# Kernel tuning notes

Measured on AMD Instinct MI355X. Metric: run time of the kernel, lower is better.

The kernel has to match this reference:

```python
import jax, jax.numpy as jnp
import numpy as np

T = 0.1  # temperature (init arg t)


def setup_inputs() -> dict:
    key = jax.random.key(0)
    k0, k1, k2, k3 = jax.random.split(key, 4)
    B, C, H, W, N = 1, 64, 256, 256, 4096
    emb_0 = jax.random.normal(k0, (B, C, H, W), dtype=jnp.float32)
    emb_1 = jax.random.normal(k1, (B, C, H, W), dtype=jnp.float32)
    # module assumes embeddings are already L2-normalized along channels
    emb_0 = emb_0 / jnp.linalg.norm(emb_0, axis=1, keepdims=True)
    emb_1 = emb_1 / jnp.linalg.norm(emb_1, axis=1, keepdims=True)
    locations_0 = jax.random.randint(k2, (B, N, 2), 0, H).astype(jnp.float32)
    locations_1 = jax.random.randint(k3, (B, N, 2), 0, H).astype(jnp.float32)
    return {"emb_0": emb_0, "emb_1": emb_1,
            "locations_0": locations_0, "locations_1": locations_1}


def reference(emb_0, emb_1, locations_0, locations_1):
    b, c, H, W = emb_0.shape  # b == 1
    n = locations_0.shape[1]
    v = H * W
    # (b, v, c)
    e0 = emb_0.reshape(b, c, v).transpose(0, 2, 1)
    e1 = emb_1.reshape(b, c, v).transpose(0, 2, 1)
    # flatten 2D coords to linear indices: strides [W, 1]
    ind_kernel = jnp.array([W, 1], dtype=jnp.float32)
    ind_0 = (jnp.floor(locations_0) @ ind_kernel).astype(jnp.int32)[0]  # (n,)
    ind_1 = (jnp.floor(locations_1) @ ind_kernel).astype(jnp.int32)[0]  # (n,)
    e0 = e0[:, ind_0, :]  # (b, n, c)
    e1 = e1[:, ind_1, :]  # (b, n, c)
    emb = jnp.concatenate([e0, e1], axis=1)  # (b, 2n, c)
    sim = jnp.einsum('bic,bjc->bij', emb, emb)  # (b, 2n, 2n)
    exp = jnp.exp(sim / T)
    sum_e = jnp.sum(exp, axis=2) - np.exp(1.0 / T)  # subtract self-similarity
    u = jnp.arange(n)
    w = u + n
    e_uv = exp[:, u, w]  # (b, n) positive pairs
    loss = -jnp.sum(jnp.log(e_uv / sum_e[:, u]) + jnp.log(e_uv / sum_e[:, w]))
    return loss / (2 * n)
```

## Files before the change

kernel.cpp:

```cpp
#include <hip/hip_runtime.h>
#include <math.h>

#define HW2     65536
#define NLOC    4096
#define NROW    8192
#define CDIM    64
#define TINV    10.0f
#define EXP10   22026.465794806718f
#define JCHUNKS 16
#define JCHUNK  512

#if __has_builtin(__builtin_amdgcn_exp2f)
#define ASCALE  14.426950408889634f
#define EXPFN(x) __builtin_amdgcn_exp2f(x)
#else
#define ASCALE  10.0f
#define EXPFN(x) __expf(x)
#endif

typedef __attribute__((ext_vector_type(8))) short bf16x8;
typedef __attribute__((ext_vector_type(4))) float f32x4;
typedef unsigned short u16;

__device__ __forceinline__ unsigned short f2bf(float f) {
  unsigned u = __builtin_bit_cast(unsigned, f);
  u += 0x7FFFu + ((u >> 16) & 1u);
  return (unsigned short)(u >> 16);
}
__device__ __forceinline__ float bf2f(unsigned u16v) {
  unsigned u = u16v << 16;
  return __builtin_bit_cast(float, u);
}

__global__ __launch_bounds__(256) void transpose_kernel(
    const float* __restrict__ emb0, const float* __restrict__ emb1,
    u16* __restrict__ embT0, u16* __restrict__ embT1) {
  __shared__ u16 T[64 * 72];
  const int tid = threadIdx.x;
  const float* emb = blockIdx.y ? emb1 : emb0;
  u16* embT        = blockIdx.y ? embT1 : embT0;
  const int w0 = blockIdx.x * 64;

#pragma unroll
  for (int q = 0; q < 4; ++q) {
    const int c = q * 16 + (tid >> 4);
    const int x = tid & 15;
    float4 v = *reinterpret_cast<const float4*>(&emb[(size_t)c * HW2 + w0 + x * 4]);
    T[(x * 4 + 0) * 72 + c] = f2bf(v.x);
    T[(x * 4 + 1) * 72 + c] = f2bf(v.y);
    T[(x * 4 + 2) * 72 + c] = f2bf(v.z);
    T[(x * 4 + 3) * 72 + c] = f2bf(v.w);
  }
  __syncthreads();
#pragma unroll
  for (int q = 0; q < 2; ++q) {
    const int w  = q * 32 + (tid >> 3);
    const int c8 = tid & 7;
    bf16x8 v = *reinterpret_cast<const bf16x8*>(&T[w * 72 + c8 * 8]);
    *reinterpret_cast<bf16x8*>(&embT[(size_t)(w0 + w) * CDIM + c8 * 8]) = v;
  }
}

__global__ __launch_bounds__(256) void gather2_kernel(
    const u16* __restrict__ embT0, const u16* __restrict__ embT1,
    const float* __restrict__ loc0, const float* __restrict__ loc1,
    u16* __restrict__ Ga, u16* __restrict__ Gb) {
  const int t = blockIdx.x * 256 + threadIdx.x;
  const int i = t >> 3;
  const int p = t & 7;
  const float* loc = (i < NLOC) ? loc0 : loc1;
  const u16*   eT  = (i < NLOC) ? embT0 : embT1;
  const int u = (i < NLOC) ? i : i - NLOC;
  const int ind = (int)floorf(loc[u * 2]) * 256 + (int)floorf(loc[u * 2 + 1]);
  bf16x8 v = *reinterpret_cast<const bf16x8*>(&eT[(size_t)ind * CDIM + p * 8]);
  *reinterpret_cast<bf16x8*>(&Gb[(size_t)i * CDIM + p * 8]) = v;
  bf16x8 vs;
#pragma unroll
  for (int e = 0; e < 8; ++e) {
    float f = bf2f((unsigned short)v[e]);
    vs[e] = (short)f2bf(f * ASCALE);
  }
  *reinterpret_cast<bf16x8*>(&Ga[(size_t)i * CDIM + p * 8]) = vs;
}

__global__ __launch_bounds__(256) void gather_kernel(
    const float* __restrict__ emb0, const float* __restrict__ emb1,
    const float* __restrict__ loc0, const float* __restrict__ loc1,
    u16* __restrict__ Ga, u16* __restrict__ Gb) {
  int t = blockIdx.x * 256 + threadIdx.x;
  int i = t >> 6;
  int c = t & 63;
  const float* loc = (i < NLOC) ? loc0 : loc1;
  const float* emb = (i < NLOC) ? emb0 : emb1;
  int u = (i < NLOC) ? i : (i - NLOC);
  int ind = (int)floorf(loc[u * 2]) * 256 + (int)floorf(loc[u * 2 + 1]);
  float v = emb[(size_t)c * HW2 + ind];
  Gb[t] = f2bf(v);
  Ga[t] = f2bf(v * ASCALE);
}

__device__ __forceinline__ void stage_tile(u16* Bs, const u16* __restrict__ Gb,
                                           int jb, int buf, int tid, int wave,
                                           int srow, int ssl) {
#pragma unroll
  for (int r = 0; r < 2; ++r) {
    const u16* src = Gb + (size_t)(jb + r * 32 + srow) * CDIM + ssl * 8;
#if __has_builtin(__builtin_amdgcn_global_load_lds)
    u16* dst = Bs + buf * 4096 + r * 2048 + wave * 512;
    __builtin_amdgcn_global_load_lds(
        (const __attribute__((address_space(1))) unsigned int*)src,
        (__attribute__((address_space(3))) unsigned int*)dst, 16, 0, 0);
#else
    bf16x8 tmp = *reinterpret_cast<const bf16x8*>(src);
    *reinterpret_cast<bf16x8*>(Bs + buf * 4096 + r * 2048 + tid * 8) = tmp;
#endif
  }
}

__global__ __launch_bounds__(256) void simsum_kernel(
    const u16* __restrict__ Ga, const u16* __restrict__ Gb,
    float* __restrict__ rowPart) {
  __shared__ u16 Bs[2 * 64 * CDIM];
  const int tid  = threadIdx.x;
  const int lane = tid & 63;
  const int wave = tid >> 6;
  const int lrow = lane & 15;
  const int kh   = lane >> 4;
  const int i0 = blockIdx.x * 128 + wave * 32;
  const int j0 = blockIdx.y * JCHUNK;

  const bf16x8* arowA =
      reinterpret_cast<const bf16x8*>(Ga + (size_t)(i0 + lrow) * CDIM + kh * 8);
  const bf16x8* arowB =
      reinterpret_cast<const bf16x8*>(Ga + (size_t)(i0 + 16 + lrow) * CDIM + kh * 8);
  bf16x8 aA0 = arowA[0], aA1 = arowA[4];
  bf16x8 aB0 = arowB[0], aB1 = arowB[4];

  const int srow = tid >> 3;
  const int ssl  = (tid & 7) ^ (srow & 7);
  const int sp0 = ((kh ^ (lrow & 7)) << 3);
  const int sp1 = (((4 + kh) ^ (lrow & 7)) << 3);

  float accA[4][4], accB[4][4];
#pragma unroll
  for (int nf = 0; nf < 4; ++nf)
#pragma unroll
    for (int r = 0; r < 4; ++r) { accA[nf][r] = 0.f; accB[nf][r] = 0.f; }

  stage_tile(Bs, Gb, j0, 0, tid, wave, srow, ssl);
  __syncthreads();

  int cur = 0;
  for (int js = 0; js < JCHUNK / 64; ++js) {
    if (js < JCHUNK / 64 - 1)
      stage_tile(Bs, Gb, j0 + (js + 1) * 64, cur ^ 1, tid, wave, srow, ssl);

    const u16* bs = Bs + cur * 4096;
#pragma unroll
    for (int nf = 0; nf < 4; ++nf) {
      const int rb = (nf * 16 + lrow) * CDIM;
      bf16x8 b0 = *reinterpret_cast<const bf16x8*>(bs + rb + sp0);
      bf16x8 b1 = *reinterpret_cast<const bf16x8*>(bs + rb + sp1);
      f32x4 z = {0.f, 0.f, 0.f, 0.f};
      f32x4 tA = __builtin_amdgcn_mfma_f32_16x16x32_bf16(aA0, b0, z, 0, 0, 0);
      tA = __builtin_amdgcn_mfma_f32_16x16x32_bf16(aA1, b1, tA, 0, 0, 0);
      f32x4 tB = __builtin_amdgcn_mfma_f32_16x16x32_bf16(aB0, b0, z, 0, 0, 0);
      tB = __builtin_amdgcn_mfma_f32_16x16x32_bf16(aB1, b1, tB, 0, 0, 0);
#pragma unroll
      for (int r = 0; r < 4; ++r) {
        accA[nf][r] += EXPFN(tA[r]);
        accB[nf][r] += EXPFN(tB[r]);
      }
    }

    __syncthreads();
    cur ^= 1;
  }

#pragma unroll
  for (int r = 0; r < 4; ++r) {
    float vA = (accA[0][r] + accA[1][r]) + (accA[2][r] + accA[3][r]);
    float vB = (accB[0][r] + accB[1][r]) + (accB[2][r] + accB[3][r]);
    vA += __shfl_xor(vA, 1, 16);
    vA += __shfl_xor(vA, 2, 16);
    vA += __shfl_xor(vA, 4, 16);
    vA += __shfl_xor(vA, 8, 16);
    vB += __shfl_xor(vB, 1, 16);
    vB += __shfl_xor(vB, 2, 16);
    vB += __shfl_xor(vB, 4, 16);
    vB += __shfl_xor(vB, 8, 16);
    if (lrow == 0) {
      rowPart[(size_t)(i0 + kh * 4 + r) * JCHUNKS + blockIdx.y] = vA;
      rowPart[(size_t)(i0 + 16 + kh * 4 + r) * JCHUNKS + blockIdx.y] = vB;
    }
  }
}

__global__ __launch_bounds__(256) void finpart_kernel(
    const u16* __restrict__ Gb, const float* __restrict__ rowPart,
    float* __restrict__ partA, float* __restrict__ partB) {
  __shared__ float sA[256];
  __shared__ float sB[256];
  const int tid = threadIdx.x, b = blockIdx.x;

  float logAcc = 0.f;
  if (tid < 128) {
    const int row = b * 128 + tid;
    float s = 0.f;
#pragma unroll
    for (int c = 0; c < JCHUNKS; ++c) s += rowPart[(size_t)row * JCHUNKS + c];
    logAcc = logf(s - EXP10);
  }
  float cross = 0.f;
  if (tid < 64) {
    const int u = b * 64 + tid;
    const unsigned* r0 = reinterpret_cast<const unsigned*>(Gb + (size_t)u * CDIM);
    const unsigned* r1 =
        reinterpret_cast<const unsigned*>(Gb + (size_t)(u + NLOC) * CDIM);
#pragma unroll
    for (int c = 0; c < 32; ++c) {
      unsigned a = r0[c], bb = r1[c];
      cross += bf2f(a & 0xffffu) * bf2f(bb & 0xffffu) + bf2f(a >> 16) * bf2f(bb >> 16);
    }
  }
  sA[tid] = logAcc;
  sB[tid] = cross;
  __syncthreads();
  for (int s = 128; s > 0; s >>= 1) {
    if (tid < s) { sA[tid] += sA[tid + s]; sB[tid] += sB[tid + s]; }
    __syncthreads();
  }
  if (tid == 0) { partA[b] = sA[0]; partB[b] = sB[0]; }
}

__global__ __launch_bounds__(64) void fin2_kernel(
    const float* __restrict__ partA, const float* __restrict__ partB,
    float* __restrict__ out) {
  const int l = threadIdx.x;
  float a = partA[l];
  float c = partB[l];
#pragma unroll
  for (int s = 1; s < 64; s <<= 1) {
    a += __shfl_xor(a, s, 64);
    c += __shfl_xor(c, s, 64);
  }
  if (l == 0) out[0] = (a - 2.0f * TINV * c) / (float)NROW;
}

extern "C" void kernel_launch(void* const* d_in, const int* in_sizes, int n_in,
                              void* d_out, int out_size, void* d_ws, size_t ws_size,
                              hipStream_t stream) {
  const float* emb0 = (const float*)d_in[0];
  const float* emb1 = (const float*)d_in[1];
  const float* loc0 = (const float*)d_in[2];
  const float* loc1 = (const float*)d_in[3];
  float* out = (float*)d_out;
  char* ws = (char*)d_ws;

  const size_t NEED = (18ull << 20) + (512ull << 10) + (8ull << 10);
  u16 *Ga, *Gb;
  float *rowPart, *partA, *partB;

  if (ws_size >= NEED) {
    u16* embT0 = (u16*)(ws);
    u16* embT1 = (u16*)(ws + (8ull << 20));
    Ga = (u16*)(ws + (16ull << 20));
    Gb = (u16*)(ws + (17ull << 20));
    rowPart = (float*)(ws + (18ull << 20));
    partA = (float*)(ws + (18ull << 20) + (512ull << 10));
    partB = partA + 64;

    dim3 tg(HW2 / 64, 2);
    transpose_kernel<<<tg, 256, 0, stream>>>(emb0, emb1, embT0, embT1);
    gather2_kernel<<<(NROW * 8) / 256, 256, 0, stream>>>(embT0, embT1, loc0, loc1,
                                                         Ga, Gb);
  } else {
    Ga = (u16*)ws;
    Gb = Ga + (size_t)NROW * CDIM;
    rowPart = (float*)(Gb + (size_t)NROW * CDIM);
    partA = rowPart + (size_t)NROW * JCHUNKS;
    partB = partA + 64;
    gather_kernel<<<(NROW * CDIM) / 256, 256, 0, stream>>>(emb0, emb1, loc0, loc1,
                                                           Ga, Gb);
  }

  dim3 grid(NROW / 128, JCHUNKS);
  simsum_kernel<<<grid, 256, 0, stream>>>(Ga, Gb, rowPart);
  finpart_kernel<<<64, 256, 0, stream>>>(Gb, rowPart, partA, partB);
  fin2_kernel<<<1, 64, 0, stream>>>(partA, partB, out);
}
```

Before: 45.53 us.

## Exploit similarity symmetry by computing only upper-triangular tile pairs

Replaces the full row-by-chunk grid with a triangular enumeration of 128x128 tile pairs, decoding (p,q) from the block index. Each off-diagonal tile contributes both its row sums and its column sums (reduced through shared memory), roughly halving MFMA and exp work. The cost is a larger partial-sum buffer (64 partials per row), extra shuffles and a shared-memory reduction, and no double-buffered pipeline inside a block.

```diff
diff --git a/kernel.cpp b/kernel.cpp
--- a/kernel.cpp
+++ b/kernel.cpp
@@ -7,8 +7,8 @@
 #define CDIM    64
 #define TINV    10.0f
 #define EXP10   22026.465794806718f
-#define JCHUNKS 16
-#define JCHUNK  512
+#define NP      64
+#define NPAIR   2080
 
 #if __has_builtin(__builtin_amdgcn_exp2f)
 #define ASCALE  14.426950408889634f
@@ -117,17 +117,30 @@
   }
 }
 
-__global__ __launch_bounds__(256) void simsum_kernel(
+__global__ __launch_bounds__(256) void simsum_tri_kernel(
     const u16* __restrict__ Ga, const u16* __restrict__ Gb,
     float* __restrict__ rowPart) {
   __shared__ u16 Bs[2 * 64 * CDIM];
+  __shared__ float colRed[4][128];
+
   const int tid  = threadIdx.x;
   const int lane = tid & 63;
   const int wave = tid >> 6;
   const int lrow = lane & 15;
   const int kh   = lane >> 4;
-  const int i0 = blockIdx.x * 128 + wave * 32;
-  const int j0 = blockIdx.y * JCHUNK;
+
+  const int b = blockIdx.x;
+  int p = (int)((129.0f - sqrtf(16641.0f - 8.0f * (float)b)) * 0.5f);
+  if (p < 0) p = 0;
+  if (p > NP - 1) p = NP - 1;
+#pragma unroll
+  for (int it = 0; it < 3; ++it) {
+    if (p > 0 && (p * NP - p * (p - 1) / 2) > b) --p;
+    else if (((p + 1) * NP - (p + 1) * p / 2) <= b) ++p;
+  }
+  const int q  = p + (b - (p * NP - p * (p - 1) / 2));
+  const int p0 = p * 128, q0 = q * 128;
+  const int i0 = p0 + wave * 32;
 
   const bf16x8* arowA =
       reinterpret_cast<const bf16x8*>(Ga + (size_t)(i0 + lrow) * CDIM + kh * 8);
@@ -138,6 +151,10 @@
 
   const int srow = tid >> 3;
   const int ssl  = (tid & 7) ^ (srow & 7);
+  stage_tile(Bs, Gb, q0,      0, tid, wave, srow, ssl);
+  stage_tile(Bs, Gb, q0 + 64, 1, tid, wave, srow, ssl);
+  __syncthreads();
+
   const int sp0 = ((kh ^ (lrow & 7)) << 3);
   const int sp1 = (((4 + kh) ^ (lrow & 7)) << 3);
 
@@ -146,16 +163,11 @@
   for (int nf = 0; nf < 4; ++nf)
 #pragma unroll
     for (int r = 0; r < 4; ++r) { accA[nf][r] = 0.f; accB[nf][r] = 0.f; }
-
-  stage_tile(Bs, Gb, j0, 0, tid, wave, srow, ssl);
-  __syncthreads();
-
-  int cur = 0;
-  for (int js = 0; js < JCHUNK / 64; ++js) {
-    if (js < JCHUNK / 64 - 1)
-      stage_tile(Bs, Gb, j0 + (js + 1) * 64, cur ^ 1, tid, wave, srow, ssl);
-
-    const u16* bs = Bs + cur * 4096;
+  float colAcc[2][4];
+
+#pragma unroll
+  for (int t = 0; t < 2; ++t) {
+    const u16* bs = Bs + t * 4096;
 #pragma unroll
     for (int nf = 0; nf < 4; ++nf) {
       const int rb = (nf * 16 + lrow) * CDIM;
@@ -166,15 +178,17 @@
       tA = __builtin_amdgcn_mfma_f32_16x16x32_bf16(aA1, b1, tA, 0, 0, 0);
       f32x4 tB = __builtin_amdgcn_mfma_f32_16x16x32_bf16(aB0, b0, z, 0, 0, 0);
       tB = __builtin_amdgcn_mfma_f32_16x16x32_bf16(aB1, b1, tB, 0, 0, 0);
+      float cp = 0.f;
 #pragma unroll
       for (int r = 0; r < 4; ++r) {
-        accA[nf][r] += EXPFN(tA[r]);
-        accB[nf][r] += EXPFN(tB[r]);
+        float eA = EXPFN(tA[r]);
+        float eB = EXPFN(tB[r]);
+        accA[nf][r] += eA;
+        accB[nf][r] += eB;
+        cp += eA + eB;
       }
-    }
-
-    __syncthreads();
-    cur ^= 1;
+      colAcc[t][nf] = cp;
+    }
   }
 
 #pragma unroll
@@ -190,8 +204,26 @@
     vB += __shfl_xor(vB, 4, 16);
     vB += __shfl_xor(vB, 8, 16);
     if (lrow == 0) {
-      rowPart[(size_t)(i0 + kh * 4 + r) * JCHUNKS + blockIdx.y] = vA;
-      rowPart[(size_t)(i0 + 16 + kh * 4 + r) * JCHUNKS + blockIdx.y] = vB;
+      rowPart[(size_t)(i0 + kh * 4 + r) * NP + q] = vA;
+      rowPart[(size_t)(i0 + 16 + kh * 4 + r) * NP + q] = vB;
+    }
+  }
+
+  if (p != q) {
+#pragma unroll
+    for (int t = 0; t < 2; ++t)
+#pragma unroll
+      for (int nf = 0; nf < 4; ++nf) {
+        float c = colAcc[t][nf];
+        c += __shfl_xor(c, 16, 64);
+        c += __shfl_xor(c, 32, 64);
+        if (kh == 0) colRed[wave][t * 64 + nf * 16 + lrow] = c;
+      }
+    __syncthreads();
+    if (tid < 128) {
+      float s = (colRed[0][tid] + colRed[1][tid]) +
+                (colRed[2][tid] + colRed[3][tid]);
+      rowPart[(size_t)(q0 + tid) * NP + p] = s;
     }
   }
 }
@@ -206,9 +238,13 @@
   float logAcc = 0.f;
   if (tid < 128) {
     const int row = b * 128 + tid;
+    const float4* rp = reinterpret_cast<const float4*>(rowPart + (size_t)row * NP);
     float s = 0.f;
 #pragma unroll
-    for (int c = 0; c < JCHUNKS; ++c) s += rowPart[(size_t)row * JCHUNKS + c];
+    for (int c = 0; c < NP / 4; ++c) {
+      float4 v = rp[c];
+      s += (v.x + v.y) + (v.z + v.w);
+    }
     logAcc = logf(s - EXP10);
   }
   float cross = 0.f;
@@ -257,7 +293,7 @@
   float* out = (float*)d_out;
   char* ws = (char*)d_ws;
 
-  const size_t NEED = (18ull << 20) + (512ull << 10) + (8ull << 10);
+  const size_t NEED = (16ull << 20) + (2ull << 20) + (2ull << 20) + (8ull << 10);
   u16 *Ga, *Gb;
   float *rowPart, *partA, *partB;
 
@@ -267,7 +303,7 @@
     Ga = (u16*)(ws + (16ull << 20));
     Gb = (u16*)(ws + (17ull << 20));
     rowPart = (float*)(ws + (18ull << 20));
-    partA = (float*)(ws + (18ull << 20) + (512ull << 10));
+    partA = (float*)(ws + (20ull << 20));
     partB = partA + 64;
 
     dim3 tg(HW2 / 64, 2);
@@ -278,14 +314,13 @@
     Ga = (u16*)ws;
     Gb = Ga + (size_t)NROW * CDIM;
     rowPart = (float*)(Gb + (size_t)NROW * CDIM);
-    partA = rowPart + (size_t)NROW * JCHUNKS;
+    partA = rowPart + (size_t)NROW * NP;
     partB = partA + 64;
     gather_kernel<<<(NROW * CDIM) / 256, 256, 0, stream>>>(emb0, emb1, loc0, loc1,
                                                            Ga, Gb);
   }
 
-  dim3 grid(NROW / 128, JCHUNKS);
-  simsum_kernel<<<grid, 256, 0, stream>>>(Ga, Gb, rowPart);
+  simsum_tri_kernel<<<NPAIR, 256, 0, stream>>>(Ga, Gb, rowPart);
   finpart_kernel<<<64, 256, 0, stream>>>(Gb, rowPart, partA, partB);
   fin2_kernel<<<1, 64, 0, stream>>>(partA, partB, out);
 }
```

Measured after the change: 38.52 us. -15.4%, faster.
